# Kernel tuning notes

Measured on AMD Instinct MI355X. Metric: run time of the kernel, lower is better.

Reference implementation:

```python
import jax, jax.numpy as jnp
import numpy as np

DIM = 3072
HEADS = 24
HEAD_DIM = 128
SEQ = 4096
BATCH = 1
EPS = 1e-6


def setup_inputs() -> dict:
    key = jax.random.key(0)
    ks = jax.random.split(key, 12)
    s = 1.0 / np.sqrt(DIM)
    return {
        "hidden_states": jax.random.normal(ks[0], (BATCH, SEQ, DIM), dtype=jnp.float32),
        "cos": jax.random.uniform(ks[1], (SEQ, HEAD_DIM), dtype=jnp.float32, minval=-1.0, maxval=1.0),
        "sin": jax.random.uniform(ks[2], (SEQ, HEAD_DIM), dtype=jnp.float32, minval=-1.0, maxval=1.0),
        "Wq": jax.random.normal(ks[3], (DIM, HEADS * HEAD_DIM), dtype=jnp.float32) * s,
        "bq": jax.random.normal(ks[4], (HEADS * HEAD_DIM,), dtype=jnp.float32) * 0.02,
        "Wk": jax.random.normal(ks[5], (DIM, HEADS * HEAD_DIM), dtype=jnp.float32) * s,
        "bk": jax.random.normal(ks[6], (HEADS * HEAD_DIM,), dtype=jnp.float32) * 0.02,
        "Wv": jax.random.normal(ks[7], (DIM, HEADS * HEAD_DIM), dtype=jnp.float32) * s,
        "bv": jax.random.normal(ks[8], (HEADS * HEAD_DIM,), dtype=jnp.float32) * 0.02,
        "gq": jnp.ones((HEAD_DIM,), dtype=jnp.float32),
        "gk": jnp.ones((HEAD_DIM,), dtype=jnp.float32),
    }


def _rms_norm(x, g):
    # RMSNorm over last dim (head_dim), learnable scale g
    var = jnp.mean(jnp.square(x), axis=-1, keepdims=True)
    return x * jax.lax.rsqrt(var + EPS) * g


def _apply_rope(x, cos, sin):
    # x: [B, S, H, D]; cos/sin: [S, D]. Interleaved-pair rotation (Flux style).
    xr = x.reshape(*x.shape[:-1], HEAD_DIM // 2, 2)
    x_rot = jnp.stack((-xr[..., 1], xr[..., 0]), axis=-1).reshape(x.shape)
    c = cos[None, :, None, :]
    s = sin[None, :, None, :]
    return x * c + x_rot * s


def reference(hidden_states, cos, sin, Wq, bq, Wk, bk, Wv, bv, gq, gk):
    B, S, _ = hidden_states.shape
    q = (hidden_states @ Wq + bq).reshape(B, S, HEADS, HEAD_DIM)
    k = (hidden_states @ Wk + bk).reshape(B, S, HEADS, HEAD_DIM)
    v = (hidden_states @ Wv + bv).reshape(B, S, HEADS, HEAD_DIM)
    q = _apply_rope(_rms_norm(q, gq), cos, sin)
    k = _apply_rope(_rms_norm(k, gk), cos, sin)
    scale = 1.0 / jnp.sqrt(jnp.asarray(HEAD_DIM, dtype=q.dtype))
    scores = jnp.einsum("bqhd,bkhd->bhqk", q, k) * scale  # [B, H, S, S]
    probs = jax.nn.softmax(scores, axis=-1)
    out = jnp.einsum("bhqk,bkhd->bqhd", probs, v)  # [B, S, H, D]
    return out.reshape(B, S, HEADS * HEAD_DIM)
```

## Files before the change

kernel.cpp:

```cpp
#include <hip/hip_runtime.h>
#include <hip/hip_bf16.h>
#include <stdint.h>

#define DIM 3072
#define SEQ 4096
#define NH 24
#define HD 128

typedef __hip_bfloat16 bf16;
typedef __bf16 bfv8 __attribute__((ext_vector_type(8)));
typedef float f32x4 __attribute__((ext_vector_type(4)));
typedef float f32x16 __attribute__((ext_vector_type(16)));
typedef unsigned short us4 __attribute__((ext_vector_type(4)));
typedef unsigned short us8 __attribute__((ext_vector_type(8)));

template <int N> struct ic { static constexpr int value = N; };

__device__ __forceinline__ void async16(void* lds, const void* g) {
  __builtin_amdgcn_global_load_lds((const __attribute__((address_space(1))) void*)g,
                                   (__attribute__((address_space(3))) void*)lds, 16, 0, 0);
}

__device__ __forceinline__ unsigned short f2bf(float f) {
  unsigned int u = __builtin_bit_cast(unsigned int, f);
  u += 0x7fffu + ((u >> 16) & 1u);
  return (unsigned short)(u >> 16);
}
__device__ __forceinline__ float bf2f(unsigned short b) {
  return __builtin_bit_cast(float, (unsigned int)b << 16);
}
__device__ __forceinline__ unsigned int cvtpk(float lo, float hi) {
  unsigned int r;
  asm("v_cvt_pk_bf16_f32 %0, %1, %2" : "=v"(r) : "v"(lo), "v"(hi));
  return r;
}
__device__ __forceinline__ void pl32swap(unsigned int& a, unsigned int& b) {
  asm volatile("v_permlane32_swap_b32 %0, %1" : "+v"(a), "+v"(b));
}

#define MFMA16(a, b, c) __builtin_amdgcn_mfma_f32_16x16x32_bf16((a), (b), (c), 0, 0, 0)
#define MFMA32(a, b, c) __builtin_amdgcn_mfma_f32_32x32x16_bf16((a), (b), (c), 0, 0, 0)

__global__ __launch_bounds__(256) void k_cast(const float4* __restrict__ in,
                                              us4* __restrict__ o, int n4) {
  int i = blockIdx.x * 256 + threadIdx.x;
  if (i >= n4) return;
  float4 v = in[i];
  us4 r;
  r.x = f2bf(v.x); r.y = f2bf(v.y); r.z = f2bf(v.z); r.w = f2bf(v.w);
  o[i] = r;
}

__global__ __launch_bounds__(256) void k_transW(const float* __restrict__ W0,
    const float* __restrict__ W1, const float* __restrict__ W2,
    unsigned short* __restrict__ T0, unsigned short* __restrict__ T1,
    unsigned short* __restrict__ T2) {
  int z = blockIdx.z;
  const float* W = (z == 0) ? W0 : (z == 1) ? W1 : W2;
  unsigned short* T = (z == 0) ? T0 : (z == 1) ? T1 : T2;
  int kb = blockIdx.y * 64;
  int nb = blockIdx.x * 64;
  __shared__ float tile[64 * 64];
  int t = threadIdx.x;
#pragma unroll
  for (int p = 0; p < 4; ++p) {
    int cid = p * 256 + t;
    int row = cid >> 4, c4 = cid & 15;
    int slot = (c4 + (row >> 3)) & 15;
    float4 v = *(const float4*)&W[(size_t)(kb + row) * DIM + nb + c4 * 4];
    *(float4*)&tile[row * 64 + slot * 4] = v;
  }
  __syncthreads();
#pragma unroll
  for (int p = 0; p < 2; ++p) {
    int cid = p * 256 + t;
    int nl = cid >> 3, c8 = cid & 7;
    us8 o;
#pragma unroll
    for (int j = 0; j < 8; ++j) {
      int k = c8 * 8 + j;
      int slot = ((nl >> 2) + (k >> 3)) & 15;
      o[j] = f2bf(tile[k * 64 + slot * 4 + (nl & 3)]);
    }
    *(us8*)&T[(size_t)(nb + nl) * DIM + kb + c8 * 8] = o;
  }
}

__global__ __launch_bounds__(256, 2) void k_gemm(const unsigned short* __restrict__ A,
    const unsigned short* __restrict__ B0, const unsigned short* __restrict__ B1,
    const unsigned short* __restrict__ B2, const float* __restrict__ c0,
    const float* __restrict__ c1, const float* __restrict__ c2,
    unsigned short* __restrict__ o0, unsigned short* __restrict__ o1,
    unsigned short* __restrict__ o2) {
  const int z = blockIdx.z;
  const unsigned short* Bt = (z == 0) ? B0 : (z == 1) ? B1 : B2;
  const float* bias = (z == 0) ? c0 : (z == 1) ? c1 : c2;
  unsigned short* outp = (z == 0) ? o0 : (z == 1) ? o1 : o2;
  const int nb = blockIdx.x * 128;
  const int mb = blockIdx.y * 128;
  const int t = threadIdx.x;
  const int w = t >> 6, l = t & 63;
  const int wr = w >> 1, wc = w & 1;
  const int lq = l & 15, lg = l >> 4;
  __shared__ unsigned short lA[128 * 64];
  __shared__ unsigned short lB[128 * 64];
  f32x4 acc[4][4];
#pragma unroll
  for (int i = 0; i < 4; ++i)
#pragma unroll
    for (int j = 0; j < 4; ++j) acc[i][j] = (f32x4){0.f, 0.f, 0.f, 0.f};

  for (int kb = 0; kb < DIM; kb += 64) {
    __syncthreads();
#pragma unroll
    for (int r = 0; r < 4; ++r) {
      int row = (w * 4 + r) * 8 + (l >> 3);
      int sl = (l & 7) ^ (row & 7);
      async16(&lA[(w * 4 + r) * 512], A + (size_t)(mb + row) * DIM + kb + sl * 8);
      async16(&lB[(w * 4 + r) * 512], Bt + (size_t)(nb + row) * DIM + kb + sl * 8);
    }
    __syncthreads();
#pragma unroll
    for (int kc = 0; kc < 2; ++kc) {
      bfv8 af[4], bfv[4];
#pragma unroll
      for (int mf = 0; mf < 4; ++mf) {
        int row = wr * 64 + mf * 16 + lq;
        af[mf] = *(const bfv8*)&lA[row * 64 + (((kc * 4 + lg) ^ (row & 7)) * 8)];
      }
#pragma unroll
      for (int nf = 0; nf < 4; ++nf) {
        int row = wc * 64 + nf * 16 + lq;
        bfv[nf] = *(const bfv8*)&lB[row * 64 + (((kc * 4 + lg) ^ (row & 7)) * 8)];
      }
#pragma unroll
      for (int mf = 0; mf < 4; ++mf)
#pragma unroll
        for (int nf = 0; nf < 4; ++nf)
          acc[mf][nf] = MFMA16(af[mf], bfv[nf], acc[mf][nf]);
    }
  }
#pragma unroll
  for (int nf = 0; nf < 4; ++nf) {
    int n = nb + wc * 64 + nf * 16 + lq;
    float bv_ = bias[n];
    int hh = n >> 7, dd = n & 127;
    unsigned short* obase = outp + (size_t)hh * SEQ * HD + dd;
#pragma unroll
    for (int mf = 0; mf < 4; ++mf) {
      int srow = mb + wr * 64 + mf * 16 + lg * 4;
#pragma unroll
      for (int r = 0; r < 4; ++r)
        obase[(size_t)(srow + r) * HD] = f2bf(acc[mf][nf][r] + bv_);
    }
  }
}

__global__ __launch_bounds__(256) void k_rmsrope(unsigned short* __restrict__ qb,
    unsigned short* __restrict__ kbuf, const float* __restrict__ cosT,
    const float* __restrict__ sinT, const float* __restrict__ gq,
    const float* __restrict__ gk) {
  int rowid = blockIdx.x * 4 + (threadIdx.x >> 6);
  int l = threadIdx.x & 63;
  int which = (rowid >= NH * SEQ) ? 1 : 0;
  int r2 = which ? rowid - NH * SEQ : rowid;
  int hh = r2 >> 12;
  int s = r2 & 4095;
  unsigned short* base = (which ? kbuf : qb) + ((size_t)hh * SEQ + s) * HD + 2 * l;
  const float* g = which ? gk : gq;
  unsigned int u = *(const unsigned int*)base;
  float x0 = bf2f((unsigned short)(u & 0xffffu));
  float x1 = bf2f((unsigned short)(u >> 16));
  float ss = x0 * x0 + x1 * x1;
#pragma unroll
  for (int o = 1; o < 64; o <<= 1) ss += __shfl_xor(ss, o);
  float rr = rsqrtf(ss * (1.0f / 128.0f) + 1e-6f);
  int d0 = 2 * l;
  float c0v = cosT[s * HD + d0], c1v = cosT[s * HD + d0 + 1];
  float s0v = sinT[s * HD + d0], s1v = sinT[s * HD + d0 + 1];
  float y0 = x0 * rr * g[d0];
  float y1 = x1 * rr * g[d0 + 1];
  float o0 = y0 * c0v - y1 * s0v;
  float o1 = y1 * c1v + y0 * s1v;
  if (!which) { o0 *= 0.1275174373f; o1 *= 0.1275174373f; }
  *(unsigned int*)base = (unsigned int)f2bf(o0) | ((unsigned int)f2bf(o1) << 16);
}

__global__ __launch_bounds__(256) void k_transV(const unsigned short* __restrict__ vb,
                                                unsigned short* __restrict__ vt) {
  int hh = blockIdx.y;
  int sb = blockIdx.x * 64;
  __shared__ unsigned short tile[64 * 128];
  int t = threadIdx.x;
#pragma unroll
  for (int p = 0; p < 4; ++p) {
    int cid = p * 256 + t;
    int row = cid >> 4, c = cid & 15;
    int slot = (c + (row >> 3)) & 15;
    us8 v = *(const us8*)&vb[((size_t)hh * SEQ + sb + row) * HD + c * 8];
    *(us8*)&tile[row * 128 + slot * 8] = v;
  }
  __syncthreads();
#pragma unroll
  for (int p = 0; p < 4; ++p) {
    int cid = p * 256 + t;
    int d = cid >> 3, c8 = cid & 7;
    us8 o;
#pragma unroll
    for (int j = 0; j < 8; ++j) {
      int s = c8 * 8 + j;
      int slot = ((d >> 3) + (s >> 3)) & 15;
      o[j] = tile[s * 128 + slot * 8 + (d & 7)];
    }
    *(us8*)&vt[((size_t)hh * HD + d) * SEQ + sb + c8 * 8] = o;
  }
}

__global__ __launch_bounds__(256, 3) void k_attn(const unsigned short* __restrict__ qg,
    const unsigned short* __restrict__ kg, const unsigned short* __restrict__ vtg,
    float* __restrict__ outp) {
  const int h = blockIdx.y;
  const int qb0 = blockIdx.x * 128;
  const int t = threadIdx.x;
  const int w = t >> 6, l = t & 63;
  const int l31 = l & 31, hi = l >> 5;

  __shared__ unsigned short lKf[2 * 4096];
  __shared__ unsigned short lVf[2 * 4096];

  bfv8 qf[8];
  {
    const unsigned short* qrow = qg + ((size_t)h * SEQ + qb0 + w * 32 + l31) * HD + hi * 8;
#pragma unroll
    for (int ks = 0; ks < 8; ++ks) qf[ks] = *(const bfv8*)(qrow + ks * 16);
  }

  int kidx[8], vidx[4][2];
#pragma unroll
  for (int ks = 0; ks < 8; ++ks)
    kidx[ks] = l31 * 128 + (((ks * 2 + hi) ^ (l31 & 7)) * 8);
#pragma unroll
  for (int dt = 0; dt < 4; ++dt)
#pragma unroll
    for (int ksub = 0; ksub < 2; ++ksub)
      vidx[dt][ksub] = (dt * 32 + l31) * 32 + ((((ksub * 2 + hi)) ^ (l31 & 3)) * 8);

  const unsigned short *kp0, *kp1, *vp0, *vp1;
  {
    int kr0 = w * 4 + (l >> 4), kr1 = 16 + kr0;
    kp0 = kg + ((size_t)h * SEQ + kr0) * HD + (((l & 15) ^ (kr0 & 7)) * 8);
    kp1 = kg + ((size_t)h * SEQ + kr1) * HD + (((l & 15) ^ (kr1 & 7)) * 8);
    int vr0 = w * 16 + (l >> 2), vr1 = 64 + vr0;
    vp0 = vtg + ((size_t)h * HD + vr0) * SEQ + (((l & 3) ^ (vr0 & 3)) * 8);
    vp1 = vtg + ((size_t)h * HD + vr1) * SEQ + (((l & 3) ^ (vr1 & 3)) * 8);
  }

#define STAGE(B)                                                        \
  do {                                                                  \
    async16(&lKf[(B) * 4096 + w * 512], kp0);        kp0 += 32 * HD;    \
    async16(&lKf[(B) * 4096 + 2048 + w * 512], kp1); kp1 += 32 * HD;    \
    async16(&lVf[(B) * 4096 + w * 512], vp0);        vp0 += 32;         \
    async16(&lVf[(B) * 4096 + 2048 + w * 512], vp1); vp1 += 32;         \
  } while (0)

  f32x16 oacc[4];
#pragma unroll
  for (int dt = 0; dt < 4; ++dt)
#pragma unroll
    for (int r = 0; r < 16; ++r) oacc[dt][r] = 0.f;
  float m_run = -1e30f, l_run = 0.f;

  STAGE(0);
  constexpr int NT = SEQ / 32;

  auto tile = [&](auto curc, int tt) {
    constexpr int CUR = decltype(curc)::value;
    __syncthreads();
    if (tt < NT - 1) STAGE(CUR ^ 1);

    f32x16 st;
#pragma unroll
    for (int r = 0; r < 16; ++r) st[r] = 0.f;
    __builtin_amdgcn_s_setprio(1);
#pragma unroll
    for (int ks = 0; ks < 8; ++ks) {
      bfv8 kf = *(const bfv8*)&lKf[CUR * 4096 + kidx[ks]];
      st = MFMA32(kf, qf[ks], st);
    }
    __builtin_amdgcn_s_setprio(0);

    float pmax = st[0];
#pragma unroll
    for (int r = 1; r < 16; ++r) pmax = fmaxf(pmax, st[r]);
    pmax = fmaxf(pmax, __shfl_xor(pmax, 32));
    if (!__all(pmax <= m_run + 10.0f)) {
      float m_new = fmaxf(m_run, pmax);
      float alpha = exp2f(m_run - m_new);
#pragma unroll
      for (int r = 0; r < 16; ++r) {
        int qr = (r & 3) + 8 * (r >> 2) + 4 * hi;
        float ar = __shfl(alpha, qr);
#pragma unroll
        for (int dt = 0; dt < 4; ++dt) oacc[dt][r] *= ar;
      }
      l_run *= alpha;
      m_run = m_new;
    }
    float lsum = 0.f;
#pragma unroll
    for (int r = 0; r < 16; ++r) {
      st[r] = exp2f(st[r] - m_run);
      lsum += st[r];
    }
    lsum += __shfl_xor(lsum, 32);
    l_run += lsum;

    bfv8 pa[2];
    {
      unsigned int a0 = cvtpk(st[0], st[1]), a1 = cvtpk(st[2], st[3]);
      unsigned int b0 = cvtpk(st[4], st[5]), b1 = cvtpk(st[6], st[7]);
      unsigned int c0 = cvtpk(st[8], st[9]), c1 = cvtpk(st[10], st[11]);
      unsigned int d0 = cvtpk(st[12], st[13]), d1 = cvtpk(st[14], st[15]);
      pl32swap(a0, b0); pl32swap(a1, b1); pl32swap(c0, d0); pl32swap(c1, d1);
      pa[0] = __builtin_bit_cast(bfv8, make_uint4(a0, a1, b0, b1));
      pa[1] = __builtin_bit_cast(bfv8, make_uint4(c0, c1, d0, d1));
    }

    __builtin_amdgcn_s_setprio(1);
#pragma unroll
    for (int dt = 0; dt < 4; ++dt)
#pragma unroll
      for (int ksub = 0; ksub < 2; ++ksub) {
        bfv8 vf = *(const bfv8*)&lVf[CUR * 4096 + vidx[dt][ksub]];
        oacc[dt] = MFMA32(pa[ksub], vf, oacc[dt]);
      }
    __builtin_amdgcn_s_setprio(0);
  };

  for (int tt = 0; tt < NT; tt += 2) {
    tile(ic<0>{}, tt);
    tile(ic<1>{}, tt + 1);
  }

  float linv = 1.0f / l_run;
#pragma unroll
  for (int r = 0; r < 16; ++r) {
    int qr = (r & 3) + 8 * (r >> 2) + 4 * hi;
    float lr = __shfl(linv, qr);
    float* orow = outp + (size_t)(qb0 + w * 32 + qr) * DIM + h * HD;
#pragma unroll
    for (int dt = 0; dt < 4; ++dt) orow[dt * 32 + l31] = oacc[dt][r] * lr;
  }
#undef STAGE
}

extern "C" void kernel_launch(void* const* d_in, const int* in_sizes, int n_in,
                              void* d_out, int out_size, void* d_ws, size_t ws_size,
                              hipStream_t stream) {
  const float* hs = (const float*)d_in[0];
  const float* cosT = (const float*)d_in[1];
  const float* sinT = (const float*)d_in[2];
  const float* Wq = (const float*)d_in[3];
  const float* bq = (const float*)d_in[4];
  const float* Wk = (const float*)d_in[5];
  const float* bk = (const float*)d_in[6];
  const float* Wv = (const float*)d_in[7];
  const float* bv = (const float*)d_in[8];
  const float* gq = (const float*)d_in[9];
  const float* gk = (const float*)d_in[10];
  float* out = (float*)d_out;

  char* ws = (char*)d_ws;
  const size_t SZ_HS = (size_t)SEQ * DIM * 2;
  const size_t SZ_W = (size_t)DIM * DIM * 2;
  const size_t SZ_HEAD = (size_t)NH * SEQ * HD * 2;
  unsigned short* hsb = (unsigned short*)ws;               ws += SZ_HS;
  unsigned short* WqT = (unsigned short*)ws;               ws += SZ_W;
  unsigned short* WkT = (unsigned short*)ws;               ws += SZ_W;
  unsigned short* WvT = (unsigned short*)ws;               ws += SZ_W;
  unsigned short* q_b = (unsigned short*)ws;               ws += SZ_HEAD;
  unsigned short* k_b = (unsigned short*)ws;               ws += SZ_HEAD;
  unsigned short* v_b = (unsigned short*)ws;               ws += SZ_HEAD;
  unsigned short* vtr = (unsigned short*)ws;               ws += SZ_HEAD;

  int n4 = SEQ * DIM / 4;
  k_cast<<<dim3(n4 / 256), dim3(256), 0, stream>>>((const float4*)hs, (us4*)hsb, n4);
  k_transW<<<dim3(48, 48, 3), dim3(256), 0, stream>>>(Wq, Wk, Wv, WqT, WkT, WvT);
  k_gemm<<<dim3(24, 32, 3), dim3(256), 0, stream>>>(hsb, WqT, WkT, WvT, bq, bk, bv,
                                                    q_b, k_b, v_b);
  k_rmsrope<<<dim3(2 * NH * SEQ / 4), dim3(256), 0, stream>>>(q_b, k_b, cosT, sinT, gq, gk);
  k_transV<<<dim3(64, 24), dim3(256), 0, stream>>>(v_b, vtr);
  k_attn<<<dim3(32, 24), dim3(256), 0, stream>>>(q_b, k_b, vtr, out);
}
```

Before: 588.4 us.

## Triple-buffer K/V tiles in attention with explicit vmcnt waits

Moves the attention kernel's K/V LDS staging from double to triple buffering, prefetching two tiles ahead. It replaces the per-tile __syncthreads with a partial s_waitcnt vmcnt plus s_barrier so one tile's loads can stay in flight during compute. It also extends the LDS XOR swizzle to cut bank conflicts and turns the max and sum reductions into trees to shorten dependency chains. LDS use rises from 32KB to 48KB per block, which may lower occupancy below the launch_bounds target of 3 blocks.

```diff
diff --git a/kernel.cpp b/kernel.cpp
--- a/kernel.cpp
+++ b/kernel.cpp
@@ -225,8 +225,8 @@
   const int w = t >> 6, l = t & 63;
   const int l31 = l & 31, hi = l >> 5;
 
-  __shared__ unsigned short lKf[2 * 4096];
-  __shared__ unsigned short lVf[2 * 4096];
+  __shared__ unsigned short lKf[3 * 4096];
+  __shared__ unsigned short lVf[3 * 4096];
 
   bfv8 qf[8];
   {
@@ -238,21 +238,22 @@
   int kidx[8], vidx[4][2];
 #pragma unroll
   for (int ks = 0; ks < 8; ++ks)
-    kidx[ks] = l31 * 128 + (((ks * 2 + hi) ^ (l31 & 7)) * 8);
+    kidx[ks] = l31 * 128 + (((ks * 2 + hi) ^ (l31 & 7) ^ ((l31 >> 3) & 1)) * 8);
 #pragma unroll
   for (int dt = 0; dt < 4; ++dt)
 #pragma unroll
     for (int ksub = 0; ksub < 2; ++ksub)
-      vidx[dt][ksub] = (dt * 32 + l31) * 32 + ((((ksub * 2 + hi)) ^ (l31 & 3)) * 8);
+      vidx[dt][ksub] =
+          (dt * 32 + l31) * 32 + (((ksub * 2 + hi) ^ (l31 & 3) ^ ((l31 >> 2) & 3)) * 8);
 
   const unsigned short *kp0, *kp1, *vp0, *vp1;
   {
     int kr0 = w * 4 + (l >> 4), kr1 = 16 + kr0;
-    kp0 = kg + ((size_t)h * SEQ + kr0) * HD + (((l & 15) ^ (kr0 & 7)) * 8);
-    kp1 = kg + ((size_t)h * SEQ + kr1) * HD + (((l & 15) ^ (kr1 & 7)) * 8);
+    kp0 = kg + ((size_t)h * SEQ + kr0) * HD + (((l & 15) ^ (kr0 & 7) ^ ((kr0 >> 3) & 1)) * 8);
+    kp1 = kg + ((size_t)h * SEQ + kr1) * HD + (((l & 15) ^ (kr1 & 7) ^ ((kr1 >> 3) & 1)) * 8);
     int vr0 = w * 16 + (l >> 2), vr1 = 64 + vr0;
-    vp0 = vtg + ((size_t)h * HD + vr0) * SEQ + (((l & 3) ^ (vr0 & 3)) * 8);
-    vp1 = vtg + ((size_t)h * HD + vr1) * SEQ + (((l & 3) ^ (vr1 & 3)) * 8);
+    vp0 = vtg + ((size_t)h * HD + vr0) * SEQ + (((l & 3) ^ (vr0 & 3) ^ ((vr0 >> 2) & 3)) * 8);
+    vp1 = vtg + ((size_t)h * HD + vr1) * SEQ + (((l & 3) ^ (vr1 & 3) ^ ((vr1 >> 2) & 3)) * 8);
   }
 
 #define STAGE(B)                                                        \
@@ -271,12 +272,21 @@
   float m_run = -1e30f, l_run = 0.f;
 
   STAGE(0);
+  STAGE(1);
   constexpr int NT = SEQ / 32;
 
-  auto tile = [&](auto curc, int tt) {
-    constexpr int CUR = decltype(curc)::value;
-    __syncthreads();
-    if (tt < NT - 1) STAGE(CUR ^ 1);
+  auto tile = [&](auto bufc, auto waitc, auto stagec) {
+    constexpr int CUR = decltype(bufc)::value;
+    constexpr int WAITN = decltype(waitc)::value;
+    constexpr int DOSTAGE = decltype(stagec)::value;
+    if constexpr (WAITN == 4)
+      asm volatile("s_waitcnt vmcnt(4)" ::: "memory");
+    else
+      asm volatile("s_waitcnt vmcnt(0)" ::: "memory");
+    __builtin_amdgcn_s_barrier();
+    __builtin_amdgcn_sched_barrier(0);
+    if constexpr (DOSTAGE) STAGE((CUR + 2) % 3);
+    __builtin_amdgcn_sched_barrier(0);
 
     f32x16 st;
 #pragma unroll
@@ -289,9 +299,12 @@
     }
     __builtin_amdgcn_s_setprio(0);
 
-    float pmax = st[0];
-#pragma unroll
-    for (int r = 1; r < 16; ++r) pmax = fmaxf(pmax, st[r]);
+    float mx01 = fmaxf(st[0], st[1]), mx23 = fmaxf(st[2], st[3]);
+    float mx45 = fmaxf(st[4], st[5]), mx67 = fmaxf(st[6], st[7]);
+    float mx89 = fmaxf(st[8], st[9]), mxab = fmaxf(st[10], st[11]);
+    float mxcd = fmaxf(st[12], st[13]), mxef = fmaxf(st[14], st[15]);
+    float pmax = fmaxf(fmaxf(fmaxf(mx01, mx23), fmaxf(mx45, mx67)),
+                       fmaxf(fmaxf(mx89, mxab), fmaxf(mxcd, mxef)));
     pmax = fmaxf(pmax, __shfl_xor(pmax, 32));
     if (!__all(pmax <= m_run + 10.0f)) {
       float m_new = fmaxf(m_run, pmax);
@@ -306,12 +319,13 @@
       l_run *= alpha;
       m_run = m_new;
     }
-    float lsum = 0.f;
-#pragma unroll
-    for (int r = 0; r < 16; ++r) {
-      st[r] = exp2f(st[r] - m_run);
-      lsum += st[r];
-    }
+#pragma unroll
+    for (int r = 0; r < 16; ++r) st[r] = exp2f(st[r] - m_run);
+    float s01 = st[0] + st[1], s23 = st[2] + st[3];
+    float s45 = st[4] + st[5], s67 = st[6] + st[7];
+    float s89 = st[8] + st[9], sab = st[10] + st[11];
+    float scd = st[12] + st[13], sef = st[14] + st[15];
+    float lsum = ((s01 + s23) + (s45 + s67)) + ((s89 + sab) + (scd + sef));
     lsum += __shfl_xor(lsum, 32);
     l_run += lsum;
 
@@ -337,10 +351,13 @@
     __builtin_amdgcn_s_setprio(0);
   };
 
-  for (int tt = 0; tt < NT; tt += 2) {
-    tile(ic<0>{}, tt);
-    tile(ic<1>{}, tt + 1);
-  }
+  for (int it = 0; it < 42; ++it) {
+    tile(ic<0>{}, ic<4>{}, ic<1>{});
+    tile(ic<1>{}, ic<4>{}, ic<1>{});
+    tile(ic<2>{}, ic<4>{}, ic<1>{});
+  }
+  tile(ic<0>{}, ic<4>{}, ic<0>{});
+  tile(ic<1>{}, ic<0>{}, ic<0>{});
 
   float linv = 1.0f / l_run;
 #pragma unroll
```

Result: no change. 586.4 us (-0.3%).
